# Kernel optimization log

Measured on AMD Instinct MI355X. Metric: run time of the kernel, lower is better.

The kernel has to match this reference:

```python
import jax, jax.numpy as jnp
import numpy as np

K = 3        # attention kernel size
PAD = 1      # padding
C = 20       # out_channels (hidden_dim_1)
HALF = C // 2
POOL = 4     # MaxPool2d((1, 4))
OUT_DIM = 80


def setup_inputs() -> dict:
    key = jax.random.key(0)
    ks = jax.random.split(key, 8)
    T, D = 1024, 1280
    lin_in = C * D // POOL  # 6400
    return {
        "feature": jax.random.normal(ks[0], (T, D), jnp.float32),
        "wq": jax.random.normal(ks[1], (C, 1), jnp.float32),
        "wk": jax.random.normal(ks[2], (C, 1), jnp.float32),
        "wv": jax.random.normal(ks[3], (C, 1), jnp.float32),
        "rel_h": jax.random.normal(ks[4], (HALF, K), jnp.float32),
        "rel_w": jax.random.normal(ks[5], (HALF, K), jnp.float32),
        "dense_w": jax.random.normal(ks[6], (OUT_DIM, lin_in), jnp.float32) * 0.02,
        "dense_b": jax.random.normal(ks[7], (OUT_DIM,), jnp.float32) * 0.02,
    }


def reference(feature, wq, wk, wv, rel_h, rel_w, dense_w, dense_b):
    T, D = feature.shape
    W = D // POOL
    # MaxPool2d((1, POOL)) over last dim of [1,1,T,D]
    x = feature.reshape(T, W, POOL).max(axis=-1)[None, None]  # [1,1,T,W]

    # 1x1 convs (in_channels=1) are just channel outer products
    q = jnp.einsum('bihw,oi->bohw', x, wq)                    # [1,C,T,W]
    xp = jnp.pad(x, ((0, 0), (0, 0), (PAD, PAD), (PAD, PAD)))
    k = jnp.einsum('bihw,oi->bohw', xp, wk)                   # [1,C,T+2,W+2]
    v = jnp.einsum('bihw,oi->bohw', xp, wv)

    # unfold(2,K,1).unfold(3,K,1) -> windows flattened as (i_h*K + i_w)
    def windows(t):
        return jnp.stack([t[:, :, i:i + T, j:j + W]
                          for i in range(K) for j in range(K)], axis=-1)  # [1,C,T,W,K*K]

    k_win = windows(k)
    v_win = windows(v)

    # relative positional bias: first HALF channels get rel_h (varies along h),
    # second HALF get rel_w (varies along w); flattened to K*K in (h,w) order
    rel = jnp.concatenate([
        jnp.broadcast_to(rel_h[:, :, None], (HALF, K, K)),
        jnp.broadcast_to(rel_w[:, None, :], (HALF, K, K)),
    ], axis=0).reshape(C, K * K)
    k_win = k_win + rel[None, :, None, None, :]

    attn = jax.nn.softmax(q[..., None] * k_win, axis=-1)      # [1,C,T,W,9]
    out = jnp.sum(attn * v_win, axis=-1)                      # [1,C,T,W]
    out = jax.nn.relu(out)

    # torch: transpose(0,1) -> [C,1,T,W] then view(-1, C*W): channel-major flatten
    flat = out[0].reshape(-1, C * W)                          # [T, C*W]
    y = flat @ dense_w.T + dense_b                            # [T, OUT_DIM]
    # torch: stack -> [T,1,OUT], transpose(0,1) -> [1,T,OUT]
    return y[None, :, :]
```

## Files before the change

kernel.cpp:

```cpp
#include <hip/hip_runtime.h>
#include <hip/hip_bf16.h>

#define TT   1024
#define DD   1280
#define WW   320
#define CC   20
#define HALF 10
#define TW   (TT*WW)
#define LIN  (CC*WW)
#define OUTD 80
#define NSPLIT 20
#define LOG2E 1.4426950408889634f
#define XPAD 384

#define POOL_BLOCKS (TW/256)
#define CVT_BLOCKS  ((OUTD*LIN)/(256*8))

typedef __attribute__((ext_vector_type(4))) float f32x4;
typedef __attribute__((ext_vector_type(8))) short bf16x8;

__device__ __forceinline__ ushort f2bf(float v) {
    unsigned u = __float_as_uint(v);
    u += 0x7FFFu + ((u >> 16) & 1u);
    return (ushort)(u >> 16);
}

__device__ __forceinline__ unsigned pk_bf16(float lo, float hi) {
    unsigned r;
    asm("v_cvt_pk_bf16_f32 %0, %1, %2" : "=v"(r) : "v"(lo), "v"(hi));
    return r;
}

__global__ __launch_bounds__(256) void k_prep(const float* __restrict__ f,
                                              float* __restrict__ x,
                                              const float* __restrict__ dw,
                                              ushort* __restrict__ dwb) {
    int b = blockIdx.x;
    if (b < POOL_BLOCKS) {
        int idx = b * 256 + threadIdx.x;
        float4 v = reinterpret_cast<const float4*>(f)[idx];
        x[idx] = fmaxf(fmaxf(v.x, v.y), fmaxf(v.z, v.w));
    } else {
        int i = ((b - POOL_BLOCKS) * 256 + threadIdx.x) * 8;
        float4 a = reinterpret_cast<const float4*>(dw + i)[0];
        float4 c = reinterpret_cast<const float4*>(dw + i)[1];
        reinterpret_cast<ushort4*>(dwb + i)[0] =
            make_ushort4(f2bf(a.x), f2bf(a.y), f2bf(a.z), f2bf(a.w));
        reinterpret_cast<ushort4*>(dwb + i)[1] =
            make_ushort4(f2bf(c.x), f2bf(c.y), f2bf(c.z), f2bf(c.w));
    }
}

template<bool ISH>
__device__ __forceinline__ uint2 attn_group(const float xr[3][6], float qk,
                                            float r0, float r1, float r2, float vv) {
    float G[3][6];
    #pragma unroll
    for (int dt = 0; dt < 3; ++dt) {
        float rdt = (dt == 0) ? r0 : ((dt == 1) ? r1 : r2);
        #pragma unroll
        for (int idx = 0; idx < 6; ++idx)
            G[dt][idx] = ISH ? fmaf(qk, xr[dt][idx], rdt) : (qk * xr[dt][idx]);
    }
    float o[4];
    #pragma unroll
    for (int p = 0; p < 4; ++p) {
        float xc = xr[1][p + 1];
        float s[9];
        if (ISH) {
            #pragma unroll
            for (int i = 0; i < 9; ++i) s[i] = xc * G[i / 3][p + i % 3];
        } else {
            float bb0 = r0 * xc, bb1 = r1 * xc, bb2 = r2 * xc;
            #pragma unroll
            for (int i = 0; i < 9; ++i) {
                float bbw = ((i % 3) == 0) ? bb0 : (((i % 3) == 1) ? bb1 : bb2);
                s[i] = fmaf(xc, G[i / 3][p + i % 3], bbw);
            }
        }
        float m = fmaxf(fmaxf(fmaxf(fmaxf(s[0], s[1]), s[2]),
                              fmaxf(fmaxf(s[3], s[4]), s[5])),
                        fmaxf(fmaxf(s[6], s[7]), s[8]));
        float den0 = 0.f, den1 = 0.f, num0 = 0.f, num1 = 0.f;
        #pragma unroll
        for (int i = 0; i < 9; ++i) {
            float e = __builtin_amdgcn_exp2f(s[i] - m);
            if (i & 1) { den1 += e; num1 = fmaf(e, xr[i / 3][p + i % 3], num1); }
            else       { den0 += e; num0 = fmaf(e, xr[i / 3][p + i % 3], num0); }
        }
        float den = den0 + den1, num = num0 + num1;
        o[p] = fmaxf(vv * (num * __builtin_amdgcn_rcpf(den)), 0.0f);
    }
    return make_uint2(pk_bf16(o[0], o[1]), pk_bf16(o[2], o[3]));
}

__global__ __launch_bounds__(256, 5) void k_fused(const float* __restrict__ x,
                                                  const float* __restrict__ wq,
                                                  const float* __restrict__ wk,
                                                  const float* __restrict__ wv,
                                                  const float* __restrict__ rh,
                                                  const float* __restrict__ rw,
                                                  const ushort* __restrict__ dwb,
                                                  float* __restrict__ part) {
    __shared__ __align__(16) ushort alds[16][328];
    __shared__ float red[4][16][81];

    int tid = threadIdx.x;
    int mt  = blockIdx.x;
    int sp  = blockIdx.y;

    {
        int j  = tid >> 4;
        int wg = tid & 15;
        int ct = (mt * 16 + j) * 20 + sp;
        int t  = ct & 1023;
        int c  = ct >> 10;
        bool ish = (c < HALF);

        float wqc = wq[c];
        float qk  = wqc * wk[c] * LOG2E;
        float vv  = wv[c];
        const float* rp = ish ? (rh + c * 3) : (rw + (c - HALF) * 3);
        float r0 = wqc * rp[0] * LOG2E;
        float r1 = wqc * rp[1] * LOG2E;
        float r2 = wqc * rp[2] * LOG2E;

        bool rok0 = (t > 0), rok2 = (t < TT - 1);
        const float* xb0 = x + t * WW;

        for (int u = 0; u < 5; ++u) {
            int gg = wg + 16 * u;
            int w0 = gg * 4;
            float xr[3][6];
            #pragma unroll
            for (int dt = 0; dt < 3; ++dt) {
                const float* rpx = xb0 + (dt - 1) * WW + w0;
                float4 va = *reinterpret_cast<const float4*>(rpx - 4);
                float4 vb = *reinterpret_cast<const float4*>(rpx);
                float  vc = rpx[4];
                bool rok = (dt == 1) ? true : ((dt == 0) ? rok0 : rok2);
                xr[dt][0] = (rok & (gg > 0))  ? va.w : 0.f;
                xr[dt][1] = rok ? vb.x : 0.f;
                xr[dt][2] = rok ? vb.y : 0.f;
                xr[dt][3] = rok ? vb.z : 0.f;
                xr[dt][4] = rok ? vb.w : 0.f;
                xr[dt][5] = (rok & (gg < 79)) ? vc : 0.f;
            }
            uint2 res = ish ? attn_group<true >(xr, qk, r0, r1, r2, vv)
                            : attn_group<false>(xr, qk, r0, r1, r2, vv);
            *reinterpret_cast<uint2*>(&alds[j][w0]) = res;
        }
    }

    __syncthreads();

    int wave = tid >> 6;
    int lane = tid & 63;
    int r16  = lane & 15;
    int kg   = lane >> 4;

    int ks0 = (wave < 2) ? wave * 3 : 6 + (wave - 2) * 2;
    int ksn = (wave < 2) ? 3 : 2;

    const ushort* bp = dwb + (size_t)r16 * LIN + sp * 320 + kg * 8;

    f32x4 acc[5] = {};
    for (int ks = ks0; ks < ks0 + ksn; ++ks) {
        bf16x8 af = *reinterpret_cast<const bf16x8*>(&alds[r16][ks * 32 + kg * 8]);
        #pragma unroll
        for (int jj = 0; jj < 5; ++jj) {
            bf16x8 bfr = *reinterpret_cast<const bf16x8*>(bp + ks * 32 + (size_t)jj * 16 * LIN);
            acc[jj] = __builtin_amdgcn_mfma_f32_16x16x32_bf16(af, bfr, acc[jj], 0, 0, 0);
        }
    }

    #pragma unroll
    for (int jj = 0; jj < 5; ++jj)
        #pragma unroll
        for (int r = 0; r < 4; ++r)
            red[wave][kg * 4 + r][jj * 16 + r16] = acc[jj][r];
    __syncthreads();

    float* pp = part + (size_t)sp * TT * OUTD + (size_t)(mt * 16) * OUTD;
    #pragma unroll
    for (int i2 = tid; i2 < 16 * 80; i2 += 256) {
        int row = i2 / 80, col = i2 % 80;
        pp[i2] = (red[0][row][col] + red[1][row][col]) +
                 (red[2][row][col] + red[3][row][col]);
    }
}

__global__ __launch_bounds__(256) void k_reduce(const float* __restrict__ part,
                                                const float* __restrict__ bias,
                                                float* __restrict__ out) {
    int idx4 = (blockIdx.x * 256 + threadIdx.x) * 4;
    int o = idx4 % OUTD;
    float4 s = *reinterpret_cast<const float4*>(bias + o);
    #pragma unroll
    for (int sp = 0; sp < NSPLIT; ++sp) {
        float4 p = *reinterpret_cast<const float4*>(part + (size_t)sp * TT * OUTD + idx4);
        s.x += p.x; s.y += p.y; s.z += p.z; s.w += p.w;
    }
    *reinterpret_cast<float4*>(out + idx4) = s;
}

extern "C" void kernel_launch(void* const* d_in, const int* in_sizes, int n_in,
                              void* d_out, int out_size, void* d_ws, size_t ws_size,
                              hipStream_t stream) {
    const float* feature = (const float*)d_in[0];
    const float* wq      = (const float*)d_in[1];
    const float* wk      = (const float*)d_in[2];
    const float* wv      = (const float*)d_in[3];
    const float* rel_h   = (const float*)d_in[4];
    const float* rel_w   = (const float*)d_in[5];
    const float* dense_w = (const float*)d_in[6];
    const float* dense_b = (const float*)d_in[7];
    float* out = (float*)d_out;

    float*  ws   = (float*)d_ws;
    float*  x    = ws + XPAD;
    ushort* dwb  = (ushort*)(ws + 2 * XPAD + TW);
    float*  part = (float*)(dwb + (size_t)OUTD * LIN);

    k_prep  <<<POOL_BLOCKS + CVT_BLOCKS, 256, 0, stream>>>(feature, x, dense_w, dwb);
    k_fused <<<dim3(TT/16, NSPLIT), 256, 0, stream>>>(x, wq, wk, wv, rel_h, rel_w, dwb, part);
    k_reduce<<<(TT*OUTD)/(256*4), 256, 0, stream>>>(part, dense_b, out);
}
```

Measured before the change: 33.14 us.

## Fold split-K reduction into fused kernel via atomics and pre-swizzle dense weights

Removes the separate reduction kernel and the partial-sum buffer. Each split block now atomically adds its tile into the output, with bias added by split 0, after a memset zeroes the output. The bf16 weight conversion also writes weights in MFMA fragment order, so each lane's B loads become contiguous 16-byte reads instead of strided rows. This trades a kernel launch and a partial-buffer round trip for 20-way atomic contention per output element, an extra memset, and a summation order that is no longer deterministic.

```diff
diff --git a/kernel.cpp b/kernel.cpp
--- a/kernel.cpp
+++ b/kernel.cpp
@@ -41,12 +41,20 @@
         float4 v = reinterpret_cast<const float4*>(f)[idx];
         x[idx] = fmaxf(fmaxf(v.x, v.y), fmaxf(v.z, v.w));
     } else {
-        int i = ((b - POOL_BLOCKS) * 256 + threadIdx.x) * 8;
-        float4 a = reinterpret_cast<const float4*>(dw + i)[0];
-        float4 c = reinterpret_cast<const float4*>(dw + i)[1];
-        reinterpret_cast<ushort4*>(dwb + i)[0] =
+        int q = (b - POOL_BLOCKS) * 256 + threadIdx.x;
+        int r16 = q & 15;
+        int kg  = (q >> 4) & 3;
+        int z   = q >> 6;
+        int jj  = z % 5;
+        int y   = z / 5;
+        int ks  = y % 10;
+        int sp  = y / 10;
+        const float* src = dw + (size_t)(jj * 16 + r16) * LIN + sp * 320 + ks * 32 + kg * 8;
+        float4 a = reinterpret_cast<const float4*>(src)[0];
+        float4 c = reinterpret_cast<const float4*>(src)[1];
+        reinterpret_cast<ushort4*>(dwb + (size_t)q * 8)[0] =
             make_ushort4(f2bf(a.x), f2bf(a.y), f2bf(a.z), f2bf(a.w));
-        reinterpret_cast<ushort4*>(dwb + i)[1] =
+        reinterpret_cast<ushort4*>(dwb + (size_t)q * 8)[1] =
             make_ushort4(f2bf(c.x), f2bf(c.y), f2bf(c.z), f2bf(c.w));
     }
 }
@@ -101,7 +109,8 @@
                                                   const float* __restrict__ rh,
                                                   const float* __restrict__ rw,
                                                   const ushort* __restrict__ dwb,
-                                                  float* __restrict__ part) {
+                                                  const float* __restrict__ bias,
+                                                  float* __restrict__ out) {
     __shared__ __align__(16) ushort alds[16][328];
     __shared__ float red[4][16][81];
 
@@ -162,14 +171,13 @@
     int ks0 = (wave < 2) ? wave * 3 : 6 + (wave - 2) * 2;
     int ksn = (wave < 2) ? 3 : 2;
 
-    const ushort* bp = dwb + (size_t)r16 * LIN + sp * 320 + kg * 8;
-
     f32x4 acc[5] = {};
     for (int ks = ks0; ks < ks0 + ksn; ++ks) {
         bf16x8 af = *reinterpret_cast<const bf16x8*>(&alds[r16][ks * 32 + kg * 8]);
+        const ushort* bp = dwb + (size_t)(((sp * 10 + ks) * 5) * 64 + lane) * 8;
         #pragma unroll
         for (int jj = 0; jj < 5; ++jj) {
-            bf16x8 bfr = *reinterpret_cast<const bf16x8*>(bp + ks * 32 + (size_t)jj * 16 * LIN);
+            bf16x8 bfr = *reinterpret_cast<const bf16x8*>(bp + (size_t)jj * 512);
             acc[jj] = __builtin_amdgcn_mfma_f32_16x16x32_bf16(af, bfr, acc[jj], 0, 0, 0);
         }
     }
@@ -181,27 +189,15 @@
             red[wave][kg * 4 + r][jj * 16 + r16] = acc[jj][r];
     __syncthreads();
 
-    float* pp = part + (size_t)sp * TT * OUTD + (size_t)(mt * 16) * OUTD;
+    float* op = out + (size_t)(mt * 16) * OUTD;
     #pragma unroll
     for (int i2 = tid; i2 < 16 * 80; i2 += 256) {
         int row = i2 / 80, col = i2 % 80;
-        pp[i2] = (red[0][row][col] + red[1][row][col]) +
-                 (red[2][row][col] + red[3][row][col]);
-    }
-}
-
-__global__ __launch_bounds__(256) void k_reduce(const float* __restrict__ part,
-                                                const float* __restrict__ bias,
-                                                float* __restrict__ out) {
-    int idx4 = (blockIdx.x * 256 + threadIdx.x) * 4;
-    int o = idx4 % OUTD;
-    float4 s = *reinterpret_cast<const float4*>(bias + o);
-    #pragma unroll
-    for (int sp = 0; sp < NSPLIT; ++sp) {
-        float4 p = *reinterpret_cast<const float4*>(part + (size_t)sp * TT * OUTD + idx4);
-        s.x += p.x; s.y += p.y; s.z += p.z; s.w += p.w;
-    }
-    *reinterpret_cast<float4*>(out + idx4) = s;
+        float v = (red[0][row][col] + red[1][row][col]) +
+                  (red[2][row][col] + red[3][row][col]);
+        if (sp == 0) v += bias[col];
+        atomicAdd(&op[i2], v);
+    }
 }
 
 extern "C" void kernel_launch(void* const* d_in, const int* in_sizes, int n_in,
@@ -220,9 +216,9 @@
     float*  ws   = (float*)d_ws;
     float*  x    = ws + XPAD;
     ushort* dwb  = (ushort*)(ws + 2 * XPAD + TW);
-    float*  part = (float*)(dwb + (size_t)OUTD * LIN);
-
-    k_prep  <<<POOL_BLOCKS + CVT_BLOCKS, 256, 0, stream>>>(feature, x, dense_w, dwb);
-    k_fused <<<dim3(TT/16, NSPLIT), 256, 0, stream>>>(x, wq, wk, wv, rel_h, rel_w, dwb, part);
-    k_reduce<<<(TT*OUTD)/(256*4), 256, 0, stream>>>(part, dense_b, out);
-}
+
+    hipMemsetAsync(out, 0, (size_t)TT * OUTD * sizeof(float), stream);
+    k_prep <<<POOL_BLOCKS + CVT_BLOCKS, 256, 0, stream>>>(feature, x, dense_w, dwb);
+    k_fused<<<dim3(TT/16, NSPLIT), 256, 0, stream>>>(x, wq, wk, wv, rel_h, rel_w,
+                                                     dwb, dense_b, out);
+}
```

New measurement: 32.47 us. 2.0% less time.
